# Kernel tuning notes

Hardware: AMD Instinct MI355X
Metric: run time of the kernel (lower is better)

The kernel has to match this reference:

```python
import jax, jax.numpy as jnp
import numpy as np

N_NODES = 100000


def gcn_conv(x, edge_index, edge_weight, W, b):
    # PyG GCNConv: x' = D^{-1/2} (A + I) D^{-1/2} (x W) + b
    n = x.shape[0]
    h = x @ W  # [N, out]
    src, dst = edge_index[0], edge_index[1]
    loop = jnp.arange(n, dtype=edge_index.dtype)
    src2 = jnp.concatenate([src, loop])
    dst2 = jnp.concatenate([dst, loop])
    ew2 = jnp.concatenate([edge_weight, jnp.ones((n,), dtype=x.dtype)])
    deg = jax.ops.segment_sum(ew2, dst2, num_segments=n)  # weighted in-degree incl self-loop
    dinv = jnp.where(deg > 0, jax.lax.rsqrt(deg), 0.0)
    norm = dinv[src2] * ew2 * dinv[dst2]  # [E+N]
    msgs = h[src2] * norm[:, None]  # gather + scale
    out = jax.ops.segment_sum(msgs, dst2, num_segments=n)  # scatter-add at targets
    return out + b


def setup_inputs() -> dict:
    key = jax.random.key(0)
    k1, k2, k3, k4, k5 = jax.random.split(key, 5)
    F_in, H, C = 128, 64, 16
    E = 1600000
    x = jax.random.normal(k1, (N_NODES, F_in), dtype=jnp.float32)
    edge_index = jax.random.randint(k2, (2, E), 0, N_NODES, dtype=jnp.int64)
    edge_weights = jax.random.uniform(k3, (E,), dtype=jnp.float32)
    W1 = jax.random.normal(k4, (F_in, H), dtype=jnp.float32) * (1.0 / np.sqrt(F_in))
    b1 = jnp.zeros((H,), dtype=jnp.float32)
    W2 = jax.random.normal(k5, (H, C), dtype=jnp.float32) * (1.0 / np.sqrt(H))
    b2 = jnp.zeros((C,), dtype=jnp.float32)
    return {"x": x, "edge_index": edge_index, "edge_weights": edge_weights,
            "W1": W1, "b1": b1, "W2": W2, "b2": b2}


def reference(x, edge_index, edge_weights, W1, b1, W2, b2):
    h = gcn_conv(x, edge_index, edge_weights, W1, b1)
    h = jax.nn.relu(h)
    # dropout inactive at inference (F.dropout with training=False is identity)
    h = gcn_conv(h, edge_index, edge_weights, W2, b2)
    return jax.nn.log_softmax(h, axis=1)
```

## Files before the change

### kernel.cpp

```cpp
#include <hip/hip_runtime.h>


#define BSHIFT 7
#define BNODES 128
#define NBUK_MAX 1024
#define CSTR 16
#define CAP 3072
#define CHUNK 8192
#define EPB 8
#define P1_TB 1024

typedef unsigned short ushort_t;
typedef unsigned int uint_t;
typedef unsigned short us4 __attribute__((ext_vector_type(4)));

__device__ inline ushort_t f2bf(float f) {
    uint_t u = __float_as_uint(f);
    return (ushort_t)((u + 0x7FFF + ((u >> 16) & 1)) >> 16);
}
__device__ inline float bf2f(ushort_t b) {
    return __uint_as_float(((uint_t)b) << 16);
}

__global__ __launch_bounds__(1024) void k_binit(int* __restrict__ bcur, int nbuk) {
    int t = threadIdx.x;
    if (t < nbuk) bcur[t * CSTR] = t * CAP;
}

__global__ __launch_bounds__(1024) void k_p1(const int* __restrict__ src,
                                             const int* __restrict__ dst,
                                             const float* __restrict__ ew,
                                             int* __restrict__ bcur,
                                             int2* __restrict__ tmp, int E, int nbuk) {
    __shared__ int lcnt[NBUK_MAX];
    __shared__ int lbase[NBUK_MAX];
    const int t = threadIdx.x;
    const int base = blockIdx.x * CHUNK;
    for (int j = t; j < nbuk; j += P1_TB) lcnt[j] = 0;
    __syncthreads();
    int d_r[EPB];
#pragma unroll
    for (int k = 0; k < EPB; ++k) {
        int e = base + k * P1_TB + t;
        int d = (e < E) ? dst[e] : -1;
        d_r[k] = d;
        if (d >= 0) atomicAdd(&lcnt[d >> BSHIFT], 1);
    }
    __syncthreads();
    for (int j = t; j < nbuk; j += P1_TB) {
        int c = lcnt[j];
        lbase[j] = c ? atomicAdd(&bcur[j * CSTR], c) : 0;
        lcnt[j] = 0;
    }
    __syncthreads();
#pragma unroll
    for (int k = 0; k < EPB; ++k) {
        int d = d_r[k];
        if (d < 0) continue;
        int e = base + k * P1_TB + t;
        int b = d >> BSHIFT;
        int p = lbase[b] + atomicAdd(&lcnt[b], 1);
        if (p >= nbuk * CAP) continue;
        int2 pk;
        pk.x = src[e] | ((d & (BNODES - 1)) << 17);
        pk.y = __float_as_int(ew[e]);
        tmp[p] = pk;
    }
}

__global__ __launch_bounds__(1024) void k_pscan(const int* __restrict__ bcur,
                                                int* __restrict__ boff, int nbuk) {
    __shared__ int lds[1024];
    const int t = threadIdx.x;
    int v = (t < nbuk) ? (bcur[t * CSTR] - t * CAP) : 0;
    lds[t] = v;
    __syncthreads();
    for (int off = 1; off < 1024; off <<= 1) {
        int u = (t >= off) ? lds[t - off] : 0;
        __syncthreads();
        lds[t] += u;
        __syncthreads();
    }
    if (t < nbuk) boff[t] = lds[t] - v;
    if (t == nbuk - 1) boff[nbuk] = lds[t];
}

__global__ __launch_bounds__(256) void k_p2(const int2* __restrict__ tmp,
                                            const int* __restrict__ bcur,
                                            const int* __restrict__ boff,
                                            int* __restrict__ rowptr,
                                            int2* __restrict__ epack,
                                            float* __restrict__ dinv,
                                            int n, int nbuk) {
    __shared__ int cnt[BNODES];
    __shared__ int pos[BNODES];
    __shared__ float degf[BNODES];
    const int b = blockIdx.x, t = threadIdx.x;
    const int node0 = b << BSHIFT;
    if (t < BNODES) { cnt[t] = 0; degf[t] = 0.f; }
    __syncthreads();
    const int lo_t = b * CAP, hi_t = bcur[b * CSTR];
    const int outb = boff[b];
    for (int i = lo_t + t; i < hi_t; i += 256) {
        int2 pk = tmp[i];
        int dlo = (pk.x >> 17) & (BNODES - 1);
        atomicAdd(&cnt[dlo], 1);
        atomicAdd(&degf[dlo], __int_as_float(pk.y));
    }
    __syncthreads();
    int own = (t < BNODES) ? cnt[t] : 0;
    if (t < BNODES) pos[t] = own;
    __syncthreads();
    for (int off = 1; off < BNODES; off <<= 1) {
        int u = (t < BNODES && t >= off) ? pos[t - off] : 0;
        __syncthreads();
        if (t < BNODES) pos[t] += u;
        __syncthreads();
    }
    if (t < BNODES) {
        int excl = pos[t] - own;
        int node = node0 + t;
        if (node < n) {
            rowptr[node] = outb + excl;
            dinv[node] = rsqrtf(1.0f + degf[t]);
        }
        pos[t] = excl;
    }
    if (b == nbuk - 1 && t == 0) rowptr[n] = outb + (hi_t - lo_t);
    __syncthreads();
    for (int i = lo_t + t; i < hi_t; i += 256) {
        int2 pk = tmp[i];
        int dlo = (pk.x >> 17) & (BNODES - 1);
        int p = outb + atomicAdd(&pos[dlo], 1);
        int2 o;
        o.x = pk.x & 0x1FFFF;
        o.y = pk.y;
        epack[p] = o;
    }
}

__global__ __launch_bounds__(256) void k_gemm1(const float* __restrict__ x,
                                               const float* __restrict__ W,
                                               const float* __restrict__ dinv,
                                               ushort_t* __restrict__ h, int n) {
    __shared__ float Ws[64 * 64];
    __shared__ float xs[64][68];
    const int t = threadIdx.x;
    const int node0 = blockIdx.x * 64;
    const int fg = t & 15;
    const int ng = t >> 4;
    float4 acc[4];
#pragma unroll
    for (int j = 0; j < 4; ++j) acc[j] = make_float4(0.f, 0.f, 0.f, 0.f);
    const float4* Ws4 = (const float4*)Ws;
    for (int half = 0; half < 2; ++half) {
        __syncthreads();
        for (int i = t; i < 64 * 64; i += 256) Ws[i] = W[half * 64 * 64 + i];
        for (int i = t; i < 64 * 16; i += 256) {
            int nn = i >> 4, q = i & 15;
            int node = node0 + nn;
            float4 v = (node < n) ? ((const float4*)x)[(size_t)node * 32 + half * 16 + q]
                                  : make_float4(0.f, 0.f, 0.f, 0.f);
            *(float4*)&xs[nn][q * 4] = v;
        }
        __syncthreads();
#pragma unroll 4
        for (int kb = 0; kb < 16; ++kb) {
            float4 xv[4];
#pragma unroll
            for (int j = 0; j < 4; ++j)
                xv[j] = *(const float4*)&xs[ng + 16 * j][kb * 4];
            float4 w0 = Ws4[(kb * 4 + 0) * 16 + fg];
            float4 w1 = Ws4[(kb * 4 + 1) * 16 + fg];
            float4 w2 = Ws4[(kb * 4 + 2) * 16 + fg];
            float4 w3 = Ws4[(kb * 4 + 3) * 16 + fg];
#pragma unroll
            for (int j = 0; j < 4; ++j) {
                acc[j].x = fmaf(xv[j].x, w0.x, acc[j].x);
                acc[j].y = fmaf(xv[j].x, w0.y, acc[j].y);
                acc[j].z = fmaf(xv[j].x, w0.z, acc[j].z);
                acc[j].w = fmaf(xv[j].x, w0.w, acc[j].w);
                acc[j].x = fmaf(xv[j].y, w1.x, acc[j].x);
                acc[j].y = fmaf(xv[j].y, w1.y, acc[j].y);
                acc[j].z = fmaf(xv[j].y, w1.z, acc[j].z);
                acc[j].w = fmaf(xv[j].y, w1.w, acc[j].w);
                acc[j].x = fmaf(xv[j].z, w2.x, acc[j].x);
                acc[j].y = fmaf(xv[j].z, w2.y, acc[j].y);
                acc[j].z = fmaf(xv[j].z, w2.z, acc[j].z);
                acc[j].w = fmaf(xv[j].z, w2.w, acc[j].w);
                acc[j].x = fmaf(xv[j].w, w3.x, acc[j].x);
                acc[j].y = fmaf(xv[j].w, w3.y, acc[j].y);
                acc[j].z = fmaf(xv[j].w, w3.z, acc[j].z);
                acc[j].w = fmaf(xv[j].w, w3.w, acc[j].w);
            }
        }
    }
#pragma unroll
    for (int j = 0; j < 4; ++j) {
        int node = node0 + ng + 16 * j;
        if (node < n) {
            float di = dinv[node];
            us4 pk;
            pk.x = f2bf(acc[j].x * di);
            pk.y = f2bf(acc[j].y * di);
            pk.z = f2bf(acc[j].z * di);
            pk.w = f2bf(acc[j].w * di);
            *(us4*)(h + (size_t)node * 64 + fg * 4) = pk;
        }
    }
}

__global__ __launch_bounds__(256) void k_agg64(const ushort_t* __restrict__ h,
                                               const int* __restrict__ rowptr,
                                               const int2* __restrict__ ep,
                                               const float* __restrict__ dinv,
                                               float* __restrict__ agg, int n) {
    const int node = __builtin_amdgcn_readfirstlane((int)((blockIdx.x * 256 + threadIdx.x) >> 6));
    const int lane = threadIdx.x & 63;
    if (node >= n) return;
    const float di = dinv[node];
    const int lo = rowptr[node], hi = rowptr[node + 1];
    const ushort_t* __restrict__ hl = h + lane;
    float accE = 0.f;
    int i = lo;
    if (i + 8 <= hi) {
        int2 pb[8], nb[8];
#pragma unroll
        for (int k = 0; k < 8; ++k) pb[k] = ep[i + k];
        i += 8;
        for (; i + 8 <= hi; i += 8) {
#pragma unroll
            for (int k = 0; k < 8; ++k) nb[k] = ep[i + k];
            float v[8];
#pragma unroll
            for (int k = 0; k < 8; ++k) v[k] = bf2f(hl[(size_t)pb[k].x * 64]);
#pragma unroll
            for (int k = 0; k < 8; ++k) accE = fmaf(v[k], __int_as_float(pb[k].y), accE);
#pragma unroll
            for (int k = 0; k < 8; ++k) pb[k] = nb[k];
        }
        {
            float v[8];
#pragma unroll
            for (int k = 0; k < 8; ++k) v[k] = bf2f(hl[(size_t)pb[k].x * 64]);
#pragma unroll
            for (int k = 0; k < 8; ++k) accE = fmaf(v[k], __int_as_float(pb[k].y), accE);
        }
    }
    for (; i < hi; ++i) {
        int2 p = ep[i];
        accE = fmaf(bf2f(hl[(size_t)p.x * 64]), __int_as_float(p.y), accE);
    }
    float self = bf2f(hl[(size_t)node * 64]);
    agg[(size_t)node * 64 + lane] = di * (accE + self);
}

__global__ __launch_bounds__(256) void k_agg16(const ushort_t* __restrict__ h,
                                               const int* __restrict__ rowptr,
                                               const int2* __restrict__ ep,
                                               const float* __restrict__ dinv,
                                               float* __restrict__ agg, int n) {
    const int node = (blockIdx.x * 256 + threadIdx.x) >> 4;
    const int lane = threadIdx.x & 15;
    if (node >= n) return;
    const float di = dinv[node];
    float accE = 0.f;
    const int lo = rowptr[node], hi = rowptr[node + 1];
    int i = lo;
    for (; i + 3 < hi; i += 4) {
        int2 p0 = ep[i], p1 = ep[i + 1], p2 = ep[i + 2], p3 = ep[i + 3];
        float v0 = bf2f(h[(size_t)p0.x * 16 + lane]);
        float v1 = bf2f(h[(size_t)p1.x * 16 + lane]);
        float v2 = bf2f(h[(size_t)p2.x * 16 + lane]);
        float v3 = bf2f(h[(size_t)p3.x * 16 + lane]);
        accE = fmaf(v0, __int_as_float(p0.y), accE);
        accE = fmaf(v1, __int_as_float(p1.y), accE);
        accE = fmaf(v2, __int_as_float(p2.y), accE);
        accE = fmaf(v3, __int_as_float(p3.y), accE);
    }
    for (; i < hi; ++i) {
        int2 p = ep[i];
        accE = fmaf(bf2f(h[(size_t)p.x * 16 + lane]), __int_as_float(p.y), accE);
    }
    float self = bf2f(h[(size_t)node * 16 + lane]);
    agg[(size_t)node * 16 + lane] = di * (accE + self);
}

__global__ __launch_bounds__(256) void k_gemm2(const float* __restrict__ a,
                                               const float* __restrict__ W,
                                               const float* __restrict__ b1,
                                               const float* __restrict__ dinv,
                                               ushort_t* __restrict__ h2, int n) {
    __shared__ float Ws[64 * 16];
    __shared__ float xs[32][68];
    const int t = threadIdx.x;
    for (int i = t; i < 64 * 16; i += 256) Ws[i] = W[i];
    const int node0 = blockIdx.x * 32;
    for (int i = t; i < 32 * 64; i += 256) {
        int nn = i >> 6, kk = i & 63;
        int node = node0 + nn;
        xs[nn][kk] = (node < n) ? fmaxf(a[(size_t)node * 64 + kk] + b1[kk], 0.0f) : 0.0f;
    }
    __syncthreads();
    const int f = t & 15;
    const int ng = t >> 4;
    float a0 = 0.f, a1 = 0.f;
#pragma unroll 4
    for (int k = 0; k < 64; ++k) {
        float wv = Ws[k * 16 + f];
        a0 = fmaf(xs[ng][k], wv, a0);
        a1 = fmaf(xs[ng + 16][k], wv, a1);
    }
    if (node0 + ng < n)
        h2[(size_t)(node0 + ng) * 16 + f] = f2bf(a0 * dinv[node0 + ng]);
    if (node0 + ng + 16 < n)
        h2[(size_t)(node0 + ng + 16) * 16 + f] = f2bf(a1 * dinv[node0 + ng + 16]);
}

__global__ void k_logsoftmax(float* __restrict__ out, const float* __restrict__ b2, int n) {
    int i = blockIdx.x * blockDim.x + threadIdx.x;
    if (i >= n) return;
    const size_t base = (size_t)i * 16;
    float v[16];
#pragma unroll
    for (int f = 0; f < 16; ++f) v[f] = out[base + f] + b2[f];
    float m = v[0];
#pragma unroll
    for (int f = 1; f < 16; ++f) m = fmaxf(m, v[f]);
    float s = 0.f;
#pragma unroll
    for (int f = 0; f < 16; ++f) s += __expf(v[f] - m);
    float lse = __logf(s);
#pragma unroll
    for (int f = 0; f < 16; ++f) out[base + f] = v[f] - m - lse;
}

extern "C" void kernel_launch(void* const* d_in, const int* in_sizes, int n_in,
                              void* d_out, int out_size, void* d_ws, size_t ws_size,
                              hipStream_t stream) {
    const float* x  = (const float*)d_in[0];
    const int*   ei = (const int*)d_in[1];
    const float* ew = (const float*)d_in[2];
    const float* W1 = (const float*)d_in[3];
    const float* b1 = (const float*)d_in[4];
    const float* W2 = (const float*)d_in[5];
    const float* b2 = (const float*)d_in[6];
    float* out = (float*)d_out;

    const int n = in_sizes[0] / 128;
    const int E = in_sizes[2];
    const int* srcv = ei;
    const int* dstv = ei + E;
    const int nbuk = (n + BNODES - 1) >> BSHIFT;

    float* wsf = (float*)d_ws;
    size_t off = 0;
    float* dinv = wsf + off; off += n;
    ushort_t* h1b = (ushort_t*)(wsf + off); off += (size_t)n * 32;
    float* agg1 = wsf + off; off += (size_t)n * 64;
    off = (off + 1) & ~(size_t)1;
    int2* epack = (int2*)(wsf + off); off += (size_t)E * 2;
    int* rowptr = (int*)(wsf + off); off += n + 1;
    int* boff_d = (int*)(wsf + off); off += NBUK_MAX + 1;
    int* bcur   = (int*)(wsf + off); off += (size_t)NBUK_MAX * CSTR;
    int2* tmp   = (int2*)agg1;

    const int TB = 256;

    k_binit<<<1, 1024, 0, stream>>>(bcur, nbuk);
    k_p1<<<(E + CHUNK - 1) / CHUNK, P1_TB, 0, stream>>>(srcv, dstv, ew, bcur, tmp, E, nbuk);
    k_pscan<<<1, 1024, 0, stream>>>(bcur, boff_d, nbuk);
    k_p2<<<nbuk, TB, 0, stream>>>(tmp, bcur, boff_d, rowptr, epack, dinv, n, nbuk);

    k_gemm1<<<(n + 63) / 64, TB, 0, stream>>>(x, W1, dinv, h1b, n);
    k_agg64<<<(n * 64 + TB - 1) / TB, TB, 0, stream>>>(h1b, rowptr, epack, dinv, agg1, n);

    k_gemm2<<<(n + 31) / 32, TB, 0, stream>>>(agg1, W2, b1, dinv, h1b, n);
    k_agg16<<<(n * 16 + TB - 1) / TB, TB, 0, stream>>>(h1b, rowptr, epack, dinv, out, n);

    k_logsoftmax<<<(n + TB - 1) / TB, TB, 0, stream>>>(out, b2, n);
}
```

Baseline: 292.2 us.

## Fuse layer-2 GEMM into first aggregation and log-softmax into second

The first aggregation kernel now applies bias and ReLU, then multiplies by W2 (held in shared memory) using wave shuffles, and writes bf16 layer-2 features directly. This removes the fp32 agg1 round trip and the separate gemm2 launch. The second aggregation kernel computes log-softmax in-register with 16-lane shuffle reductions, removing the logsoftmax kernel and its extra read/write of the output. The cost is extra shuffle and LDS work per node inside the gather kernel, plus a W2 load and barrier in every block.

```diff
diff --git a/kernel.cpp b/kernel.cpp
--- a/kernel.cpp
+++ b/kernel.cpp
@@ -210,13 +210,19 @@
     }
 }
 
-__global__ __launch_bounds__(256) void k_agg64(const ushort_t* __restrict__ h,
-                                               const int* __restrict__ rowptr,
-                                               const int2* __restrict__ ep,
-                                               const float* __restrict__ dinv,
-                                               float* __restrict__ agg, int n) {
-    const int node = __builtin_amdgcn_readfirstlane((int)((blockIdx.x * 256 + threadIdx.x) >> 6));
-    const int lane = threadIdx.x & 63;
+__global__ __launch_bounds__(256) void k_agg64f(const ushort_t* __restrict__ h,
+                                                const int* __restrict__ rowptr,
+                                                const int2* __restrict__ ep,
+                                                const float* __restrict__ dinv,
+                                                const float* __restrict__ W2,
+                                                const float* __restrict__ b1,
+                                                ushort_t* __restrict__ h2, int n) {
+    __shared__ float W2s[64 * 16];
+    const int t = threadIdx.x;
+    for (int i = t; i < 64 * 16; i += 256) W2s[i] = W2[i];
+    __syncthreads();
+    const int node = __builtin_amdgcn_readfirstlane((int)((blockIdx.x * 256 + t) >> 6));
+    const int lane = t & 63;
     if (node >= n) return;
     const float di = dinv[node];
     const int lo = rowptr[node], hi = rowptr[node + 1];
@@ -252,14 +258,28 @@
         accE = fmaf(bf2f(hl[(size_t)p.x * 64]), __int_as_float(p.y), accE);
     }
     float self = bf2f(hl[(size_t)node * 64]);
-    agg[(size_t)node * 64 + lane] = di * (accE + self);
-}
-
-__global__ __launch_bounds__(256) void k_agg16(const ushort_t* __restrict__ h,
-                                               const int* __restrict__ rowptr,
-                                               const int2* __restrict__ ep,
-                                               const float* __restrict__ dinv,
-                                               float* __restrict__ agg, int n) {
+    float r = di * (accE + self);
+    float av = fmaxf(r + b1[lane], 0.0f);
+    const int f = lane & 15;
+    const int q = lane >> 4;
+    float p = 0.f;
+#pragma unroll
+    for (int kk = 0; kk < 16; ++kk) {
+        int k = q * 16 + kk;
+        float ak = __shfl(av, k, 64);
+        p = fmaf(ak, W2s[k * 16 + f], p);
+    }
+    p += __shfl_xor(p, 16, 64);
+    p += __shfl_xor(p, 32, 64);
+    if (lane < 16) h2[(size_t)node * 16 + f] = f2bf(p * di);
+}
+
+__global__ __launch_bounds__(256) void k_agg16f(const ushort_t* __restrict__ h,
+                                                const int* __restrict__ rowptr,
+                                                const int2* __restrict__ ep,
+                                                const float* __restrict__ dinv,
+                                                const float* __restrict__ b2,
+                                                float* __restrict__ out, int n) {
     const int node = (blockIdx.x * 256 + threadIdx.x) >> 4;
     const int lane = threadIdx.x & 15;
     if (node >= n) return;
@@ -283,56 +303,19 @@
         accE = fmaf(bf2f(h[(size_t)p.x * 16 + lane]), __int_as_float(p.y), accE);
     }
     float self = bf2f(h[(size_t)node * 16 + lane]);
-    agg[(size_t)node * 16 + lane] = di * (accE + self);
-}
-
-__global__ __launch_bounds__(256) void k_gemm2(const float* __restrict__ a,
-                                               const float* __restrict__ W,
-                                               const float* __restrict__ b1,
-                                               const float* __restrict__ dinv,
-                                               ushort_t* __restrict__ h2, int n) {
-    __shared__ float Ws[64 * 16];
-    __shared__ float xs[32][68];
-    const int t = threadIdx.x;
-    for (int i = t; i < 64 * 16; i += 256) Ws[i] = W[i];
-    const int node0 = blockIdx.x * 32;
-    for (int i = t; i < 32 * 64; i += 256) {
-        int nn = i >> 6, kk = i & 63;
-        int node = node0 + nn;
-        xs[nn][kk] = (node < n) ? fmaxf(a[(size_t)node * 64 + kk] + b1[kk], 0.0f) : 0.0f;
-    }
-    __syncthreads();
-    const int f = t & 15;
-    const int ng = t >> 4;
-    float a0 = 0.f, a1 = 0.f;
-#pragma unroll 4
-    for (int k = 0; k < 64; ++k) {
-        float wv = Ws[k * 16 + f];
-        a0 = fmaf(xs[ng][k], wv, a0);
-        a1 = fmaf(xs[ng + 16][k], wv, a1);
-    }
-    if (node0 + ng < n)
-        h2[(size_t)(node0 + ng) * 16 + f] = f2bf(a0 * dinv[node0 + ng]);
-    if (node0 + ng + 16 < n)
-        h2[(size_t)(node0 + ng + 16) * 16 + f] = f2bf(a1 * dinv[node0 + ng + 16]);
-}
-
-__global__ void k_logsoftmax(float* __restrict__ out, const float* __restrict__ b2, int n) {
-    int i = blockIdx.x * blockDim.x + threadIdx.x;
-    if (i >= n) return;
-    const size_t base = (size_t)i * 16;
-    float v[16];
-#pragma unroll
-    for (int f = 0; f < 16; ++f) v[f] = out[base + f] + b2[f];
-    float m = v[0];
-#pragma unroll
-    for (int f = 1; f < 16; ++f) m = fmaxf(m, v[f]);
-    float s = 0.f;
-#pragma unroll
-    for (int f = 0; f < 16; ++f) s += __expf(v[f] - m);
-    float lse = __logf(s);
-#pragma unroll
-    for (int f = 0; f < 16; ++f) out[base + f] = v[f] - m - lse;
+    float v = di * (accE + self) + b2[lane];
+    float m = v;
+    m = fmaxf(m, __shfl_xor(m, 1, 64));
+    m = fmaxf(m, __shfl_xor(m, 2, 64));
+    m = fmaxf(m, __shfl_xor(m, 4, 64));
+    m = fmaxf(m, __shfl_xor(m, 8, 64));
+    float e = __expf(v - m);
+    float s = e;
+    s += __shfl_xor(s, 1, 64);
+    s += __shfl_xor(s, 2, 64);
+    s += __shfl_xor(s, 4, 64);
+    s += __shfl_xor(s, 8, 64);
+    out[(size_t)node * 16 + lane] = v - m - __logf(s);
 }
 
 extern "C" void kernel_launch(void* const* d_in, const int* in_sizes, int n_in,
@@ -364,6 +347,7 @@
     int* boff_d = (int*)(wsf + off); off += NBUK_MAX + 1;
     int* bcur   = (int*)(wsf + off); off += (size_t)NBUK_MAX * CSTR;
     int2* tmp   = (int2*)agg1;
+    ushort_t* h2b = (ushort_t*)agg1;
 
     const int TB = 256;
 
@@ -373,10 +357,9 @@
     k_p2<<<nbuk, TB, 0, stream>>>(tmp, bcur, boff_d, rowptr, epack, dinv, n, nbuk);
 
     k_gemm1<<<(n + 63) / 64, TB, 0, stream>>>(x, W1, dinv, h1b, n);
-    k_agg64<<<(n * 64 + TB - 1) / TB, TB, 0, stream>>>(h1b, rowptr, epack, dinv, agg1, n);
-
-    k_gemm2<<<(n + 31) / 32, TB, 0, stream>>>(agg1, W2, b1, dinv, h1b, n);
-    k_agg16<<<(n * 16 + TB - 1) / TB, TB, 0, stream>>>(h1b, rowptr, epack, dinv, out, n);
-
-    k_logsoftmax<<<(n + TB - 1) / TB, TB, 0, stream>>>(out, b2, n);
-}
+    k_agg64f<<<(n * 64 + TB - 1) / TB, TB, 0, stream>>>(h1b, rowptr, epack, dinv,
+                                                        W2, b1, h2b, n);
+
+    k_agg16f<<<(n * 16 + TB - 1) / TB, TB, 0, stream>>>(h2b, rowptr, epack, dinv,
+                                                        b2, out, n);
+}
```

Measured after the change: 281.1 us. 3.8% less time.
